# Kernel tuning notes

Hardware: AMD Instinct MI355X
Metric: run time of the kernel (lower is better)

Reference implementation:

```python
import jax, jax.numpy as jnp
import numpy as np
from jax import lax

EPS = 1e-5
DN = ('NCHW', 'OIHW', 'NCHW')
# torch F.pad order is (W_left, W_right, H_top, H_bottom); lax padding is ((H_lo,H_hi),(W_lo,W_hi))
PAD1 = ((1, 1), (1, 1))  # conv (3,3), pad (1,1,1,1)
PAD2 = ((1, 0), (1, 1))  # conv (2,3), pad (1,1,1,0)
PAD3 = ((1, 1), (1, 0))  # conv (3,2), pad (1,0,1,1)
PAD4 = ((1, 0), (1, 0))  # conv (2,2), pad (1,0,1,0)


def _conv(x, w, b, pad):
    y = lax.conv_general_dilated(x, w, (1, 1), pad, dimension_numbers=DN)
    return y + b[None, :, None, None]


def _bn(x, gamma, beta):
    # BatchNorm2d in training mode: biased batch stats over (N, H, W)
    m = jnp.mean(x, axis=(0, 2, 3), keepdims=True)
    v = jnp.var(x, axis=(0, 2, 3), keepdims=True)
    return (x - m) * lax.rsqrt(v + EPS) * gamma[None, :, None, None] + beta[None, :, None, None]


def _interleave(a, b, c, d):
    # a,b,c,d: [B,C,H,W] -> [B,C,2H,2W]; A->(even,even), B->(odd,even), C->(even,odd), D->(odd,odd)
    B, C, H, W = a.shape
    top = jnp.stack([a, c], axis=4).reshape(B, C, H, 2 * W)  # even rows
    bot = jnp.stack([b, d], axis=4).reshape(B, C, H, 2 * W)  # odd rows
    return jnp.stack([top, bot], axis=3).reshape(B, C, 2 * H, 2 * W)


def _unpool_as_conv(x, wA, bA, wB, bB, wC, bC, wD, bD, gamma, beta, relu):
    oA = _conv(x, wA, bA, PAD1)
    oB = _conv(x, wB, bB, PAD2)
    oC = _conv(x, wC, bC, PAD3)
    oD = _conv(x, wD, bD, PAD4)
    y = _interleave(oA, oB, oC, oD)
    y = _bn(y, gamma, beta)
    if relu:
        y = jax.nn.relu(y)
    return y


def _forward(x, w1, b1, w2, b2, w3, b3, w4, b4, w5, b5, w6, b6, w7, b7, w8, b8,
             w9, b9, g11, be11, g12, be12, g2, be2):
    out1 = _unpool_as_conv(x, w1, b1, w2, b2, w3, b3, w4, b4, g11, be11, relu=True)
    out1 = _conv(out1, w9, b9, ((1, 1), (1, 1)))
    out1 = _bn(out1, g2, be2)
    out2 = _unpool_as_conv(x, w5, b5, w6, b6, w7, b7, w8, b8, g12, be12, relu=False)
    return jax.nn.relu(out1 + out2)


def setup_inputs() -> dict:
    key = jax.random.key(0)
    B, Cin, Cout, H, W = 16, 512, 256, 32, 32
    ks = jax.random.split(key, 32)
    it = iter(ks)

    def w(shape, fan_in):
        return jax.random.normal(next(it), shape, dtype=jnp.float32) * (1.0 / np.sqrt(fan_in))

    inp = {"x": jax.random.normal(next(it), (B, Cin, H, W), dtype=jnp.float32)}
    # branch 1 convs
    inp["w1"], inp["b1"] = w((Cout, Cin, 3, 3), Cin * 9), w((Cout,), Cin * 9)
    inp["w2"], inp["b2"] = w((Cout, Cin, 2, 3), Cin * 6), w((Cout,), Cin * 6)
    inp["w3"], inp["b3"] = w((Cout, Cin, 3, 2), Cin * 6), w((Cout,), Cin * 6)
    inp["w4"], inp["b4"] = w((Cout, Cin, 2, 2), Cin * 4), w((Cout,), Cin * 4)
    # branch 2 convs
    inp["w5"], inp["b5"] = w((Cout, Cin, 3, 3), Cin * 9), w((Cout,), Cin * 9)
    inp["w6"], inp["b6"] = w((Cout, Cin, 2, 3), Cin * 6), w((Cout,), Cin * 6)
    inp["w7"], inp["b7"] = w((Cout, Cin, 3, 2), Cin * 6), w((Cout,), Cin * 6)
    inp["w8"], inp["b8"] = w((Cout, Cin, 2, 2), Cin * 4), w((Cout,), Cin * 4)
    # conv9
    inp["w9"], inp["b9"] = w((Cout, Cout, 3, 3), Cout * 9), w((Cout,), Cout * 9)
    # batchnorms
    inp["g11"], inp["be11"] = jnp.ones((Cout,), jnp.float32), jnp.zeros((Cout,), jnp.float32)
    inp["g12"], inp["be12"] = jnp.ones((Cout,), jnp.float32), jnp.zeros((Cout,), jnp.float32)
    inp["g2"], inp["be2"] = jnp.ones((Cout,), jnp.float32), jnp.zeros((Cout,), jnp.float32)
    return inp


def reference(x, w1, b1, w2, b2, w3, b3, w4, b4, w5, b5, w6, b6, w7, b7, w8, b8,
              w9, b9, g11, be11, g12, be12, g2, be2):
    return _forward(x, w1, b1, w2, b2, w3, b3, w4, b4, w5, b5, w6, b6, w7, b7, w8, b8,
                    w9, b9, g11, be11, g12, be12, g2, be2)
```

## Files before the change

kernel.cpp:

```cpp
#include <hip/hip_runtime.h>
#include <stdint.h>


typedef __bf16 bf16x8 __attribute__((ext_vector_type(8)));
typedef float floatx4 __attribute__((ext_vector_type(4)));

typedef __attribute__((address_space(3))) uint32_t lds32_t;
typedef __attribute__((address_space(1))) const uint32_t glb32_t;

__device__ __forceinline__ void load_lds16(const uint16_t* g, uint16_t* l) {
  __builtin_amdgcn_global_load_lds((glb32_t*)g, (lds32_t*)l, 16, 0, 0);
}

__device__ __forceinline__ float bf2f(uint32_t u) {
  union { uint32_t i; float f; } v;
  v.i = u << 16;
  return v.f;
}
__device__ __forceinline__ uint16_t f2bf(float f) {
  union { float f; uint32_t i; } v;
  v.f = f;
  uint32_t r = v.i + 0x7fff + ((v.i >> 16) & 1);
  return (uint16_t)(r >> 16);
}
__device__ __forceinline__ float load_in(const void* p, size_t i, bool isbf) {
  return isbf ? bf2f(((const uint16_t*)p)[i]) : ((const float*)p)[i];
}

__device__ __forceinline__ int cls_ntaps(int cls) { return cls == 0 ? 9 : (cls == 3 ? 4 : 6); }
__device__ __forceinline__ size_t cls_off(int cls) {
  return cls == 0 ? 0u : (cls == 1 ? 2359296u : (cls == 2 ? 3932160u : 5505024u));
}
__device__ __forceinline__ void cls_tap(int cls, int r, int& dy, int& dx) {
  if (cls >= 2) { dy = r >> 1; dx = r & 1; }
  else { dy = r / 3; dx = r - 3 * (r / 3); }
}

__global__ void detect_dtype(const uint32_t* __restrict__ xw, uint32_t* __restrict__ flag) {
  int t = threadIdx.x;
  int cnt = 0;
#pragma unroll
  for (int k = 0; k < 16; ++k) {
    uint32_t u = xw[t + k * 256];
    uint32_t e = (u >> 7) & 0xFF;
    cnt += (e >= 100 && e <= 140) ? 1 : 0;
  }
  __shared__ int rs[256];
  rs[t] = cnt;
  __syncthreads();
  for (int o = 128; o > 0; o >>= 1) {
    if (t < o) rs[t] += rs[t + o];
    __syncthreads();
  }
  if (t == 0) flag[0] = (rs[0] > 2048) ? 1u : 0u;
}

__global__ void pack_w_unpool(const void* wa, const void* wb, const void* wc, const void* wd,
                              const void* we, const void* wf, const void* wg, const void* wh,
                              const uint32_t* __restrict__ flag, uint16_t* __restrict__ Wp) {
  const void* ws[8] = {wa, wb, wc, wd, we, wf, wg, wh};
  const bool isbf = flag[0] != 0;
  int m = blockIdx.y;
  int kc = blockIdx.x * 256 + threadIdx.x;
  int cls, kk;
  if (kc < 4608) { cls = 0; kk = kc; }
  else if (kc < 7680) { cls = 1; kk = kc - 4608; }
  else if (kc < 10752) { cls = 2; kk = kc - 7680; }
  else { cls = 3; kk = kc - 10752; }
  int r = kk >> 9, cin = kk & 511;
  int dy, dx;
  cls_tap(cls, r, dy, dx);
  int branch = m >> 8, cout = m & 255;
  int kh = 3 - (cls & 1), kw = 3 - (cls >> 1);
  int Kcls = cls_ntaps(cls) * 512;
  float v = load_in(ws[branch * 4 + cls], (size_t)((cout * 512 + cin) * kh + dy) * kw + dx, isbf);
  Wp[cls_off(cls) + (size_t)m * Kcls + kk] = f2bf(v);
}

__global__ void pack_w9(const void* __restrict__ w9, const uint32_t* __restrict__ flag,
                        uint16_t* __restrict__ Wp9) {
  const bool isbf = flag[0] != 0;
  int m = blockIdx.y;
  int k = blockIdx.x * 256 + threadIdx.x;
  int r = k >> 8, cin = k & 255;
  int dy = r / 3, dx = r - dy * 3;
  Wp9[(size_t)m * 2304 + k] = f2bf(load_in(w9, (size_t)((m * 256 + cin) * 3 + dy) * 3 + dx, isbf));
}

__global__ void pack_bias(const void* b1, const void* b2, const void* b3, const void* b4,
                          const void* b5, const void* b6, const void* b7, const void* b8,
                          const void* b9, const uint32_t* __restrict__ flag,
                          float* __restrict__ bpk, float* __restrict__ b9pk) {
  const void* bs[8] = {b1, b2, b3, b4, b5, b6, b7, b8};
  const bool isbf = flag[0] != 0;
  int bx = blockIdx.x, t = threadIdx.x;
  if (bx < 8) {
    int cls = bx >> 1, branch = bx & 1;
    bpk[bx * 256 + t] = load_in(bs[branch * 4 + cls], t, isbf);
  } else {
    b9pk[t] = load_in(b9, t, isbf);
  }
}

__global__ void pad_x_kernel(const void* __restrict__ x, const uint32_t* __restrict__ flag,
                             uint16_t* __restrict__ xp) {
  const bool isbf = flag[0] != 0;
  int tid = blockIdx.x * 256 + threadIdx.x;
  int cg = tid & 63;
  int rem = tid >> 6;
  int j = rem & 31; rem >>= 5;
  int i = rem & 31;
  int b = rem >> 5;
  uint16_t v[8];
#pragma unroll
  for (int e = 0; e < 8; ++e) {
    int c = cg * 8 + e;
    v[e] = f2bf(load_in(x, ((size_t)(b * 512 + c) * 32 + i) * 32 + j, isbf));
  }
  *(uint4*)&xp[((size_t)(b * 34 + i + 1) * 34 + (j + 1)) * 512 + cg * 8] = *(const uint4*)v;
}

template <int CIN, int IMGW_SHIFT, int PIXB_SHIFT, int PADW, int MODE>
__global__ __launch_bounds__(256) void gemm_conv(const uint16_t* __restrict__ Wp,
                                                 const uint16_t* __restrict__ xp,
                                                 const float* __restrict__ bias,
                                                 uint16_t* __restrict__ o0,
                                                 uint16_t* __restrict__ o1) {
  constexpr int CC2 = CIN / 64;
  constexpr int IMGW = 1 << IMGW_SHIFT;
  __shared__ uint16_t As[2 * 128 * 32];
  __shared__ uint16_t Bs[2 * 128 * 32];

  const int t = threadIdx.x;
  const int wave = t >> 6, lane = t & 63;

  int cls, mtile, nt;
  if (MODE == 0) {
    cls = blockIdx.x >> 9;
    int within = blockIdx.x & 511;
    mtile = within & 3;
    nt = within >> 2;
  } else {
    cls = 0;
    mtile = blockIdx.x & 1;
    nt = blockIdx.x >> 1;
  }
  const int n0 = nt * 128;
  const int ntaps = (MODE == 0) ? cls_ntaps(cls) : 9;
  const int Krow = (MODE == 0) ? ntaps * CIN : 9 * CIN;
  const int mrow0 = mtile * 128;
  const uint16_t* Wbase = (MODE == 0) ? Wp + cls_off(cls) : Wp;

  const int chunk = lane & 3;
  const int srow = wave * 32 + (lane >> 2);

  const uint16_t* aSrc0 = Wbase + (size_t)(mrow0 + srow) * Krow + chunk * 8;
  const uint16_t* aSrc1 = aSrc0 + (size_t)16 * Krow;

  auto pixb = [&](int n) -> size_t {
    int bb = n >> PIXB_SHIFT;
    int rem = n & ((1 << PIXB_SHIFT) - 1);
    int hh = rem >> IMGW_SHIFT;
    int ww = rem & (IMGW - 1);
    return ((size_t)(bb * PADW + hh) * PADW + ww) * CIN;
  };
  const uint16_t* bSrc0 = xp + pixb(n0 + srow) + chunk * 8;
  const uint16_t* bSrc1 = xp + pixb(n0 + srow + 16) + chunk * 8;

  uint16_t* As0W = &As[(wave * 32) * 32];
  uint16_t* As1W = As0W + 128 * 32;
  uint16_t* Bs0W = &Bs[(wave * 32) * 32];
  uint16_t* Bs1W = Bs0W + 128 * 32;

  floatx4 acc[4][4];
#pragma unroll
  for (int i = 0; i < 4; ++i)
#pragma unroll
    for (int j = 0; j < 4; ++j) acc[i][j] = floatx4{0.f, 0.f, 0.f, 0.f};

  const int wm = wave >> 1, wn = wave & 1;
  const int fl = lane & 15, kg = lane >> 4;

  int kidx = 0;
  for (int r = 0; r < ntaps; ++r) {
    int dy, dx;
    if (MODE == 0) cls_tap(cls, r, dy, dx);
    else { dy = r / 3; dx = r - 3 * dy; }
    const int toff = (dy * PADW + dx) * CIN;
    for (int cc = 0; cc < CC2; ++cc) {
      load_lds16(aSrc0 + kidx, As0W);
      load_lds16(aSrc1 + kidx, As0W + 16 * 32);
      load_lds16(aSrc0 + kidx + 32, As1W);
      load_lds16(aSrc1 + kidx + 32, As1W + 16 * 32);
      const int bo = toff + cc * 64;
      load_lds16(bSrc0 + bo, Bs0W);
      load_lds16(bSrc1 + bo, Bs0W + 16 * 32);
      load_lds16(bSrc0 + bo + 32, Bs1W);
      load_lds16(bSrc1 + bo + 32, Bs1W + 16 * 32);
      __syncthreads();
#pragma unroll
      for (int h = 0; h < 2; ++h) {
        bf16x8 af[4], bfr[4];
#pragma unroll
        for (int i = 0; i < 4; ++i)
          af[i] = *(const bf16x8*)&As[h * 4096 + (wm * 64 + i * 16 + fl) * 32 + kg * 8];
#pragma unroll
        for (int j = 0; j < 4; ++j)
          bfr[j] = *(const bf16x8*)&Bs[h * 4096 + (wn * 64 + j * 16 + fl) * 32 + kg * 8];
#pragma unroll
        for (int i = 0; i < 4; ++i)
#pragma unroll
          for (int j = 0; j < 4; ++j)
            acc[i][j] = __builtin_amdgcn_mfma_f32_16x16x32_bf16(af[i], bfr[j], acc[i][j], 0, 0, 0);
      }
      __syncthreads();
      kidx += 64;
    }
  }

#pragma unroll
  for (int i = 0; i < 4; ++i) {
#pragma unroll
    for (int reg = 0; reg < 4; ++reg) {
      const int mloc = mrow0 + wm * 64 + i * 16 + kg * 4 + reg;
      if (MODE == 0) {
        const int branch = mloc >> 8, cout = mloc & 255;
        const int ey = cls & 1, ex = cls >> 1;
        const float bv = bias[cls * 512 + mloc];
        uint16_t* o = branch ? o1 : o0;
#pragma unroll
        for (int j = 0; j < 4; ++j) {
          const int n = n0 + wn * 64 + j * 16 + fl;
          const int bb = n >> 10, hh = (n >> 5) & 31, ww = n & 31;
          o[((size_t)((bb * 256 + cout) * 64 + 2 * hh + ey) << 6) + 2 * ww + ex] =
              f2bf(acc[i][j][reg] + bv);
        }
      } else {
        const float bv = bias[mloc];
#pragma unroll
        for (int j = 0; j < 4; ++j) {
          const int n = n0 + wn * 64 + j * 16 + fl;
          const int bb = n >> 12, hh = (n >> 6) & 63, ww = n & 63;
          o0[((size_t)((bb * 256 + mloc) * 64 + hh) << 6) + ww] = f2bf(acc[i][j][reg] + bv);
        }
      }
    }
  }
}

__global__ void bn_stats(const uint16_t* __restrict__ y, const void* __restrict__ gamma,
                         const void* __restrict__ beta, const uint32_t* __restrict__ flag,
                         float2* __restrict__ out) {
  const bool isbf = flag[0] != 0;
  int c = blockIdx.x, t = threadIdx.x;
  const uint32_t* yu = (const uint32_t*)y;
  float s = 0.f, s2 = 0.f;
  for (int b = 0; b < 16; ++b) {
    size_t base = (size_t)(b * 256 + c) * 2048;
#pragma unroll
    for (int k = 0; k < 8; ++k) {
      uint32_t v = yu[base + t + k * 256];
      float lo = bf2f(v & 0xffff), hi = bf2f(v >> 16);
      s += lo + hi;
      s2 += lo * lo + hi * hi;
    }
  }
  __shared__ float rs[256], rs2[256];
  rs[t] = s; rs2[t] = s2;
  __syncthreads();
  for (int off = 128; off > 0; off >>= 1) {
    if (t < off) { rs[t] += rs[t + off]; rs2[t] += rs2[t + off]; }
    __syncthreads();
  }
  if (t == 0) {
    float mean = rs[0] * (1.f / 65536.f);
    float var = rs2[0] * (1.f / 65536.f) - mean * mean;
    float scale = load_in(gamma, c, isbf) * rsqrtf(var + 1e-5f);
    float shift = load_in(beta, c, isbf) - mean * scale;
    out[c] = make_float2(scale, shift);
  }
}

__global__ void u_fill(const uint16_t* __restrict__ y1, const float2* __restrict__ st,
                       uint16_t* __restrict__ u) {
  int tid = blockIdx.x * 256 + threadIdx.x;
  int cg = tid & 31;
  int rem = tid >> 5;
  int w = rem & 63; rem >>= 6;
  int h = rem & 63;
  int b = rem >> 6;
  uint16_t v[8];
#pragma unroll
  for (int e = 0; e < 8; ++e) {
    int c = cg * 8 + e;
    float2 ab = st[c];
    float val = fmaxf(ab.x * bf2f(y1[((size_t)(b * 256 + c) * 64 + h) * 64 + w]) + ab.y, 0.f);
    v[e] = f2bf(val);
  }
  *(uint4*)&u[((size_t)(b * 66 + h + 1) * 66 + (w + 1)) * 256 + cg * 8] = *(const uint4*)v;
}

__global__ void final_kernel(const uint16_t* __restrict__ z, const uint16_t* __restrict__ y2,
                             const float2* __restrict__ st2, const float2* __restrict__ st12,
                             const uint32_t* __restrict__ flag, void* __restrict__ out) {
  const bool isbf = flag[0] != 0;
  size_t idx = ((size_t)blockIdx.x * 256 + threadIdx.x) * 8;
  int c = (int)((idx >> 12) & 255);
  float2 a2 = st2[c], a12 = st12[c];
  uint4 vz = *(const uint4*)(z + idx);
  uint4 vy = *(const uint4*)(y2 + idx);
  float r[8];
  auto proc = [&](uint32_t uz, uint32_t uy, int o) {
    r[o] = fmaxf(a2.x * bf2f(uz & 0xffff) + a2.y + a12.x * bf2f(uy & 0xffff) + a12.y, 0.f);
    r[o + 1] = fmaxf(a2.x * bf2f(uz >> 16) + a2.y + a12.x * bf2f(uy >> 16) + a12.y, 0.f);
  };
  proc(vz.x, vy.x, 0);
  proc(vz.y, vy.y, 2);
  proc(vz.z, vy.z, 4);
  proc(vz.w, vy.w, 6);
  if (isbf) {
    uint4 vo;
    vo.x = (uint32_t)f2bf(r[0]) | ((uint32_t)f2bf(r[1]) << 16);
    vo.y = (uint32_t)f2bf(r[2]) | ((uint32_t)f2bf(r[3]) << 16);
    vo.z = (uint32_t)f2bf(r[4]) | ((uint32_t)f2bf(r[5]) << 16);
    vo.w = (uint32_t)f2bf(r[6]) | ((uint32_t)f2bf(r[7]) << 16);
    *(uint4*)((uint16_t*)out + idx) = vo;
  } else {
    float4* of = (float4*)((float*)out + idx);
    of[0] = make_float4(r[0], r[1], r[2], r[3]);
    of[1] = make_float4(r[4], r[5], r[6], r[7]);
  }
}

extern "C" void kernel_launch(void* const* d_in, const int* in_sizes, int n_in,
                              void* d_out, int out_size, void* d_ws, size_t ws_size,
                              hipStream_t stream) {
  const void* x = d_in[0];
  const void *w1 = d_in[1], *b1 = d_in[2], *w2 = d_in[3], *b2 = d_in[4];
  const void *w3 = d_in[5], *b3 = d_in[6], *w4 = d_in[7], *b4 = d_in[8];
  const void *w5 = d_in[9], *b5 = d_in[10], *w6 = d_in[11], *b6 = d_in[12];
  const void *w7 = d_in[13], *b7 = d_in[14], *w8 = d_in[15], *b8 = d_in[16];
  const void *w9 = d_in[17], *b9 = d_in[18];
  const void *g11 = d_in[19], *be11 = d_in[20], *g12 = d_in[21], *be12 = d_in[22];
  const void *g2 = d_in[23], *be2 = d_in[24];

  char* ws = (char*)d_ws;
  size_t off = 0;
  auto alloc = [&](size_t bytes) -> char* {
    char* p = ws + off;
    off = (off + bytes + 255) & ~(size_t)255;
    return p;
  };
  const size_t xp_bytes = (size_t)16 * 34 * 34 * 512 * 2;
  const size_t y_bytes = (size_t)16 * 256 * 64 * 64 * 2;
  const size_t u_bytes = (size_t)16 * 66 * 66 * 256 * 2;
  const size_t Wp_bytes = (size_t)512 * 12800 * 2;

  uint32_t* flag = (uint32_t*)alloc(256);
  uint16_t* Wp9 = (uint16_t*)alloc((size_t)256 * 2304 * 2);
  float* bpk = (float*)alloc(2048 * 4);
  float* b9pk = (float*)alloc(256 * 4);
  float2* st1a = (float2*)alloc(256 * 8);
  float2* st1b = (float2*)alloc(256 * 8);
  float2* st2 = (float2*)alloc(256 * 8);
  uint16_t* y1 = (uint16_t*)alloc(y_bytes);
  uint16_t* y2 = (uint16_t*)alloc(y_bytes);
  size_t wpal = (Wp_bytes + 255) & ~(size_t)255;
  size_t region_bytes = wpal + xp_bytes;
  if (region_bytes < u_bytes) region_bytes = u_bytes;
  char* region = alloc(region_bytes);
  uint16_t* Wp = (uint16_t*)region;
  uint16_t* xp = (uint16_t*)(region + wpal);
  uint16_t* u = (uint16_t*)region;
  uint16_t* z = y1;

  detect_dtype<<<1, 256, 0, stream>>>((const uint32_t*)x, flag);

  hipMemsetAsync(xp, 0, xp_bytes, stream);

  pack_w_unpool<<<dim3(50, 512), 256, 0, stream>>>(w1, w2, w3, w4, w5, w6, w7, w8, flag, Wp);
  pack_w9<<<dim3(9, 256), 256, 0, stream>>>(w9, flag, Wp9);
  pack_bias<<<9, 256, 0, stream>>>(b1, b2, b3, b4, b5, b6, b7, b8, b9, flag, bpk, b9pk);
  pad_x_kernel<<<4096, 256, 0, stream>>>(x, flag, xp);

  gemm_conv<512, 5, 10, 34, 0><<<2048, 256, 0, stream>>>(Wp, xp, bpk, y1, y2);

  bn_stats<<<256, 256, 0, stream>>>(y1, g11, be11, flag, st1a);
  bn_stats<<<256, 256, 0, stream>>>(y2, g12, be12, flag, st1b);

  hipMemsetAsync(u, 0, u_bytes, stream);

  u_fill<<<8192, 256, 0, stream>>>(y1, st1a, u);

  gemm_conv<256, 6, 12, 66, 1><<<1024, 256, 0, stream>>>(Wp9, u, b9pk, z, nullptr);

  bn_stats<<<256, 256, 0, stream>>>(z, g2, be2, flag, st2);

  final_kernel<<<8192, 256, 0, stream>>>(z, y2, st2, st1b, flag, d_out);
}
```

Before: 663.0 us.

## Fuse BN statistics into GEMM epilogues and use LDS transposes for layout kernels

The GEMM epilogues now accumulate per-channel sum and sum-of-squares with wave shuffles and float atomics, so the separate bn_stats passes over the bf16 outputs become tiny bn_scale kernels. pad_x and u_fill are rewritten to stage one image row per block in LDS and write coalesced NHWC words, instead of doing strided 8-element gathers per thread. This removes three full reads of the conv outputs and improves memory coalescing in the transpose kernels. The cost is atomic contention in the GEMM epilogue, nondeterministic float summation order, and stats computed from fp32 values rather than from the rounded bf16 outputs.

```diff
diff --git a/kernel.cpp b/kernel.cpp
--- a/kernel.cpp
+++ b/kernel.cpp
@@ -104,20 +104,26 @@
 
 __global__ void pad_x_kernel(const void* __restrict__ x, const uint32_t* __restrict__ flag,
                              uint16_t* __restrict__ xp) {
-  const bool isbf = flag[0] != 0;
-  int tid = blockIdx.x * 256 + threadIdx.x;
-  int cg = tid & 63;
-  int rem = tid >> 6;
-  int j = rem & 31; rem >>= 5;
-  int i = rem & 31;
-  int b = rem >> 5;
-  uint16_t v[8];
-#pragma unroll
-  for (int e = 0; e < 8; ++e) {
-    int c = cg * 8 + e;
-    v[e] = f2bf(load_in(x, ((size_t)(b * 512 + c) * 32 + i) * 32 + j, isbf));
-  }
-  *(uint4*)&xp[((size_t)(b * 34 + i + 1) * 34 + (j + 1)) * 512 + cg * 8] = *(const uint4*)v;
+  __shared__ uint16_t L16[512 * 34];
+  const bool isbf = flag[0] != 0;
+  int b = blockIdx.x >> 5, h = blockIdx.x & 31, t = threadIdx.x;
+#pragma unroll
+  for (int k = 0; k < 64; ++k) {
+    int idx = t + k * 256;
+    int c = idx >> 5, j = idx & 31;
+    L16[c * 34 + j] = f2bf(load_in(x, ((size_t)(b * 512 + c) * 32 + h) * 32 + j, isbf));
+  }
+  __syncthreads();
+  uint32_t* xpu = (uint32_t*)xp;
+  size_t rowbase = ((size_t)(b * 34 + h + 1) * 34 + 1) * 256;
+#pragma unroll
+  for (int k = 0; k < 32; ++k) {
+    int flat = t + k * 256;
+    int j = flat >> 8, s = flat & 255;
+    uint32_t lo = L16[(2 * s) * 34 + j];
+    uint32_t hi = L16[(2 * s + 1) * 34 + j];
+    xpu[rowbase + (size_t)j * 256 + s] = lo | (hi << 16);
+  }
 }
 
 template <int CIN, int IMGW_SHIFT, int PIXB_SHIFT, int PADW, int MODE>
@@ -125,7 +131,8 @@
                                                  const uint16_t* __restrict__ xp,
                                                  const float* __restrict__ bias,
                                                  uint16_t* __restrict__ o0,
-                                                 uint16_t* __restrict__ o1) {
+                                                 uint16_t* __restrict__ o1,
+                                                 float* __restrict__ stat) {
   constexpr int CC2 = CIN / 64;
   constexpr int IMGW = 1 << IMGW_SHIFT;
   __shared__ uint16_t As[2 * 128 * 32];
@@ -223,6 +230,7 @@
 #pragma unroll
     for (int reg = 0; reg < 4; ++reg) {
       const int mloc = mrow0 + wm * 64 + i * 16 + kg * 4 + reg;
+      float vsum = 0.f, vsq = 0.f;
       if (MODE == 0) {
         const int branch = mloc >> 8, cout = mloc & 255;
         const int ey = cls & 1, ex = cls >> 1;
@@ -232,8 +240,18 @@
         for (int j = 0; j < 4; ++j) {
           const int n = n0 + wn * 64 + j * 16 + fl;
           const int bb = n >> 10, hh = (n >> 5) & 31, ww = n & 31;
-          o[((size_t)((bb * 256 + cout) * 64 + 2 * hh + ey) << 6) + 2 * ww + ex] =
-              f2bf(acc[i][j][reg] + bv);
+          const float v = acc[i][j][reg] + bv;
+          vsum += v; vsq += v * v;
+          o[((size_t)((bb * 256 + cout) * 64 + 2 * hh + ey) << 6) + 2 * ww + ex] = f2bf(v);
+        }
+#pragma unroll
+        for (int msk = 1; msk < 16; msk <<= 1) {
+          vsum += __shfl_xor(vsum, msk);
+          vsq += __shfl_xor(vsq, msk);
+        }
+        if (fl == 0) {
+          atomicAdd(&stat[branch * 512 + cout], vsum);
+          atomicAdd(&stat[branch * 512 + 256 + cout], vsq);
         }
       } else {
         const float bv = bias[mloc];
@@ -241,63 +259,63 @@
         for (int j = 0; j < 4; ++j) {
           const int n = n0 + wn * 64 + j * 16 + fl;
           const int bb = n >> 12, hh = (n >> 6) & 63, ww = n & 63;
-          o0[((size_t)((bb * 256 + mloc) * 64 + hh) << 6) + ww] = f2bf(acc[i][j][reg] + bv);
+          const float v = acc[i][j][reg] + bv;
+          vsum += v; vsq += v * v;
+          o0[((size_t)((bb * 256 + mloc) * 64 + hh) << 6) + ww] = f2bf(v);
+        }
+#pragma unroll
+        for (int msk = 1; msk < 16; msk <<= 1) {
+          vsum += __shfl_xor(vsum, msk);
+          vsq += __shfl_xor(vsq, msk);
+        }
+        if (fl == 0) {
+          atomicAdd(&stat[mloc], vsum);
+          atomicAdd(&stat[256 + mloc], vsq);
         }
       }
     }
   }
 }
 
-__global__ void bn_stats(const uint16_t* __restrict__ y, const void* __restrict__ gamma,
+__global__ void bn_scale(const float* __restrict__ sums, const void* __restrict__ gamma,
                          const void* __restrict__ beta, const uint32_t* __restrict__ flag,
-                         float2* __restrict__ out) {
-  const bool isbf = flag[0] != 0;
-  int c = blockIdx.x, t = threadIdx.x;
-  const uint32_t* yu = (const uint32_t*)y;
-  float s = 0.f, s2 = 0.f;
-  for (int b = 0; b < 16; ++b) {
-    size_t base = (size_t)(b * 256 + c) * 2048;
-#pragma unroll
-    for (int k = 0; k < 8; ++k) {
-      uint32_t v = yu[base + t + k * 256];
-      float lo = bf2f(v & 0xffff), hi = bf2f(v >> 16);
-      s += lo + hi;
-      s2 += lo * lo + hi * hi;
-    }
-  }
-  __shared__ float rs[256], rs2[256];
-  rs[t] = s; rs2[t] = s2;
-  __syncthreads();
-  for (int off = 128; off > 0; off >>= 1) {
-    if (t < off) { rs[t] += rs[t + off]; rs2[t] += rs2[t + off]; }
-    __syncthreads();
-  }
-  if (t == 0) {
-    float mean = rs[0] * (1.f / 65536.f);
-    float var = rs2[0] * (1.f / 65536.f) - mean * mean;
-    float scale = load_in(gamma, c, isbf) * rsqrtf(var + 1e-5f);
-    float shift = load_in(beta, c, isbf) - mean * scale;
-    out[c] = make_float2(scale, shift);
-  }
+                         float2* __restrict__ st) {
+  const bool isbf = flag[0] != 0;
+  int c = threadIdx.x;
+  float mean = sums[c] * (1.f / 65536.f);
+  float var = sums[256 + c] * (1.f / 65536.f) - mean * mean;
+  float scale = load_in(gamma, c, isbf) * rsqrtf(var + 1e-5f);
+  float shift = load_in(beta, c, isbf) - mean * scale;
+  st[c] = make_float2(scale, shift);
 }
 
 __global__ void u_fill(const uint16_t* __restrict__ y1, const float2* __restrict__ st,
                        uint16_t* __restrict__ u) {
-  int tid = blockIdx.x * 256 + threadIdx.x;
-  int cg = tid & 31;
-  int rem = tid >> 5;
-  int w = rem & 63; rem >>= 6;
-  int h = rem & 63;
-  int b = rem >> 6;
-  uint16_t v[8];
-#pragma unroll
-  for (int e = 0; e < 8; ++e) {
-    int c = cg * 8 + e;
+  __shared__ uint32_t L[256 * 33];
+  int b = blockIdx.x >> 6, h = blockIdx.x & 63, t = threadIdx.x;
+  const uint32_t* yu = (const uint32_t*)y1;
+#pragma unroll
+  for (int k = 0; k < 32; ++k) {
+    int idx = t + k * 256;
+    int c = idx >> 5, wu = idx & 31;
+    uint32_t v = yu[(size_t)(b * 256 + c) * 2048 + h * 32 + wu];
     float2 ab = st[c];
-    float val = fmaxf(ab.x * bf2f(y1[((size_t)(b * 256 + c) * 64 + h) * 64 + w]) + ab.y, 0.f);
-    v[e] = f2bf(val);
-  }
-  *(uint4*)&u[((size_t)(b * 66 + h + 1) * 66 + (w + 1)) * 256 + cg * 8] = *(const uint4*)v;
+    float lo = fmaxf(ab.x * bf2f(v & 0xffff) + ab.y, 0.f);
+    float hi = fmaxf(ab.x * bf2f(v >> 16) + ab.y, 0.f);
+    L[c * 33 + wu] = (uint32_t)f2bf(lo) | ((uint32_t)f2bf(hi) << 16);
+  }
+  __syncthreads();
+  const uint16_t* L16 = (const uint16_t*)L;
+  uint32_t* uu = (uint32_t*)u;
+  size_t rowbase = ((size_t)(b * 66 + h + 1) * 66 + 1) * 128;
+#pragma unroll
+  for (int k = 0; k < 32; ++k) {
+    int flat = t + k * 256;
+    int j = flat >> 7, s = flat & 127;
+    uint32_t lo = L16[(2 * s) * 66 + j];
+    uint32_t hi = L16[(2 * s + 1) * 66 + j];
+    uu[rowbase + (size_t)j * 128 + s] = lo | (hi << 16);
+  }
 }
 
 __global__ void final_kernel(const uint16_t* __restrict__ z, const uint16_t* __restrict__ y2,
@@ -357,6 +375,7 @@
   const size_t Wp_bytes = (size_t)512 * 12800 * 2;
 
   uint32_t* flag = (uint32_t*)alloc(256);
+  float* sums = (float*)alloc(6 * 256 * 4);
   uint16_t* Wp9 = (uint16_t*)alloc((size_t)256 * 2304 * 2);
   float* bpk = (float*)alloc(2048 * 4);
   float* b9pk = (float*)alloc(256 * 4);
@@ -373,28 +392,31 @@
   uint16_t* xp = (uint16_t*)(region + wpal);
   uint16_t* u = (uint16_t*)region;
   uint16_t* z = y1;
+  float* s1 = sums;
+  float* s2 = sums + 1024;
 
   detect_dtype<<<1, 256, 0, stream>>>((const uint32_t*)x, flag);
 
+  hipMemsetAsync(sums, 0, 6 * 256 * 4, stream);
   hipMemsetAsync(xp, 0, xp_bytes, stream);
 
   pack_w_unpool<<<dim3(50, 512), 256, 0, stream>>>(w1, w2, w3, w4, w5, w6, w7, w8, flag, Wp);
   pack_w9<<<dim3(9, 256), 256, 0, stream>>>(w9, flag, Wp9);
   pack_bias<<<9, 256, 0, stream>>>(b1, b2, b3, b4, b5, b6, b7, b8, b9, flag, bpk, b9pk);
-  pad_x_kernel<<<4096, 256, 0, stream>>>(x, flag, xp);
-
-  gemm_conv<512, 5, 10, 34, 0><<<2048, 256, 0, stream>>>(Wp, xp, bpk, y1, y2);
-
-  bn_stats<<<256, 256, 0, stream>>>(y1, g11, be11, flag, st1a);
-  bn_stats<<<256, 256, 0, stream>>>(y2, g12, be12, flag, st1b);
+  pad_x_kernel<<<512, 256, 0, stream>>>(x, flag, xp);
+
+  gemm_conv<512, 5, 10, 34, 0><<<2048, 256, 0, stream>>>(Wp, xp, bpk, y1, y2, s1);
+
+  bn_scale<<<1, 256, 0, stream>>>(s1, g11, be11, flag, st1a);
+  bn_scale<<<1, 256, 0, stream>>>(s1 + 512, g12, be12, flag, st1b);
 
   hipMemsetAsync(u, 0, u_bytes, stream);
 
-  u_fill<<<8192, 256, 0, stream>>>(y1, st1a, u);
-
-  gemm_conv<256, 6, 12, 66, 1><<<1024, 256, 0, stream>>>(Wp9, u, b9pk, z, nullptr);
-
-  bn_stats<<<256, 256, 0, stream>>>(z, g2, be2, flag, st2);
+  u_fill<<<1024, 256, 0, stream>>>(y1, st1a, u);
+
+  gemm_conv<256, 6, 12, 66, 1><<<1024, 256, 0, stream>>>(Wp9, u, b9pk, z, nullptr, s2);
+
+  bn_scale<<<1, 256, 0, stream>>>(s2, g2, be2, flag, st2);
 
   final_kernel<<<8192, 256, 0, stream>>>(z, y2, st2, st1b, flag, d_out);
 }
```

Measured after the change: 737.3 us. +11.2%, slower.
